# Performance work log

Measured on AMD Instinct MI355X. Metric: run time of the kernel, lower is better.

## Reference

```python
import jax, jax.numpy as jnp
import numpy as np

B, T, C, HEADS = 4, 2305, 384, 6
BN_EPS = 1e-5


def setup_inputs() -> dict:
    key = jax.random.key(0)
    ks = jax.random.split(key, 24)
    d = {
        'x': jax.random.normal(ks[0], (B, T, C), dtype=jnp.float32),
        'h': 48,
        'w': 48,
        # depthwise conv kernels (groups=C, no bias): OIHW with I=1
        'kq': jax.random.normal(ks[1], (C, 1, 3, 3), dtype=jnp.float32) * 0.1,
        'kk': jax.random.normal(ks[2], (C, 1, 3, 3), dtype=jnp.float32) * 0.1,
        'kv': jax.random.normal(ks[3], (C, 1, 3, 3), dtype=jnp.float32) * 0.1,
        # BatchNorm (eval mode) params per projection: gamma, beta, running_mean, running_var
        'gq': jax.random.normal(ks[4], (C,), dtype=jnp.float32) * 0.1 + 1.0,
        'bq': jax.random.normal(ks[5], (C,), dtype=jnp.float32) * 0.1,
        'mq': jax.random.normal(ks[6], (C,), dtype=jnp.float32) * 0.1,
        'vq': jax.random.uniform(ks[7], (C,), dtype=jnp.float32) + 0.5,
        'gk': jax.random.normal(ks[8], (C,), dtype=jnp.float32) * 0.1 + 1.0,
        'bk': jax.random.normal(ks[9], (C,), dtype=jnp.float32) * 0.1,
        'mk': jax.random.normal(ks[10], (C,), dtype=jnp.float32) * 0.1,
        'vk': jax.random.uniform(ks[11], (C,), dtype=jnp.float32) + 0.5,
        'gv': jax.random.normal(ks[12], (C,), dtype=jnp.float32) * 0.1 + 1.0,
        'bv': jax.random.normal(ks[13], (C,), dtype=jnp.float32) * 0.1,
        'mv': jax.random.normal(ks[14], (C,), dtype=jnp.float32) * 0.1,
        'vv': jax.random.uniform(ks[15], (C,), dtype=jnp.float32) + 0.5,
        # Linear weights, torch convention [out, in]; qkv_bias=False
        'Wq': jax.random.normal(ks[16], (C, C), dtype=jnp.float32) / np.sqrt(C),
        'Wk': jax.random.normal(ks[17], (C, C), dtype=jnp.float32) / np.sqrt(C),
        'Wv': jax.random.normal(ks[18], (C, C), dtype=jnp.float32) / np.sqrt(C),
        'Wo': jax.random.normal(ks[19], (C, C), dtype=jnp.float32) / np.sqrt(C),
        'bo': jax.random.normal(ks[20], (C,), dtype=jnp.float32) * 0.01,
    }
    return d


def _dw_bn(xi, kern, gamma, beta, mean, var, h, w):
    # xi: [B, C, h, w]; depthwise 3x3 conv, stride 1, pad 1, then eval-mode BN
    y = jax.lax.conv_general_dilated(
        xi, kern, window_strides=(1, 1), padding=((1, 1), (1, 1)),
        feature_group_count=C, dimension_numbers=('NCHW', 'OIHW', 'NCHW'))
    scale = (gamma / jnp.sqrt(var + BN_EPS))[None, :, None, None]
    y = (y - mean[None, :, None, None]) * scale + beta[None, :, None, None]
    # b c h w -> b (h w) c
    return y.transpose(0, 2, 3, 1).reshape(y.shape[0], h * w, C)


def _forward(x, kq, kk, kv, gq, bq, mq, vq, gk, bk, mk, vk, gv, bv, mv, vv,
             Wq, Wk, Wv, Wo, bo, h, w):
    b, t, c = x.shape
    scale = c ** (-0.5)  # note: dim**-0.5, NOT head_dim**-0.5 (as in source)
    cls_tok, xs = x[:, :1], x[:, 1:]
    xi = xs.reshape(b, h, w, c).transpose(0, 3, 1, 2)  # b (h w) c -> b c h w
    q = jnp.concatenate([cls_tok, _dw_bn(xi, kq, gq, bq, mq, vq, h, w)], axis=1)
    k = jnp.concatenate([cls_tok, _dw_bn(xi, kk, gk, bk, mk, vk, h, w)], axis=1)
    v = jnp.concatenate([cls_tok, _dw_bn(xi, kv, gv, bv, mv, vv, h, w)], axis=1)
    dh = c // HEADS
    q = (q @ Wq.T).reshape(b, t, HEADS, dh).transpose(0, 2, 1, 3)  # bhtd
    k = (k @ Wk.T).reshape(b, t, HEADS, dh).transpose(0, 2, 1, 3)
    v = (v @ Wv.T).reshape(b, t, HEADS, dh).transpose(0, 2, 1, 3)
    attn = jax.nn.softmax(jnp.einsum('bhld,bhtd->bhlt', q, k) * scale, axis=-1)
    out = jnp.einsum('bhlt,bhtd->bhld', attn, v)
    out = out.transpose(0, 2, 1, 3).reshape(b, t, c)
    return out @ Wo.T + bo


def reference(x, kq, kk, kv, gq, bq, mq, vq, gk, bk, mk, vk, gv, bv, mv, vv,
              Wq, Wk, Wv, Wo, bo, h, w):
    return _forward(x, kq, kk, kv, gq, bq, mq, vq, gk, bk, mk, vk, gv, bv,
                    mv, vv, Wq, Wk, Wv, Wo, bo, h, w)
```

## Files before the change

### kernel.cpp

```cpp
#include <hip/hip_runtime.h>
#include <hip/hip_bf16.h>

#define BN 4
#define TT 2305
#define CC 384
#define HH 6
#define DH 64
#define GW 48
#define BH (BN*HH)
#define TP 2368
#define TQP 2560
#define MF 9220
#define MP 9344
#define MB2 73
#define NSPL 2
#define C2 0.07362223f

typedef __hip_bfloat16 bf16;
typedef __attribute__((ext_vector_type(8))) short short8;
typedef __attribute__((ext_vector_type(4))) float floatx4;
typedef __attribute__((ext_vector_type(16))) float floatx16;

#define MFMA16(a,b,c) __builtin_amdgcn_mfma_f32_16x16x32_bf16((a),(b),(c),0,0,0)
#define MFMA32(a,b,c) __builtin_amdgcn_mfma_f32_32x32x16_bf16((a),(b),(c),0,0,0)

__device__ __forceinline__ unsigned pack2(float a, float b) {
    bf16 lo = __float2bfloat16(a);
    bf16 hi = __float2bfloat16(b);
    unsigned short ul = *reinterpret_cast<unsigned short*>(&lo);
    unsigned short uh = *reinterpret_cast<unsigned short*>(&hi);
    return (unsigned)ul | ((unsigned)uh << 16);
}
__device__ __forceinline__ float bu2f(unsigned u16) {
    unsigned v = u16 << 16;
    return *reinterpret_cast<float*>(&v);
}

__global__ __launch_bounds__(384)
void conv_bn(const float* __restrict__ x,
             const float* __restrict__ kq, const float* __restrict__ kk, const float* __restrict__ kv,
             const float* __restrict__ gq, const float* __restrict__ bq, const float* __restrict__ mq, const float* __restrict__ vq,
             const float* __restrict__ gk, const float* __restrict__ bk, const float* __restrict__ mk, const float* __restrict__ vk,
             const float* __restrict__ gv, const float* __restrict__ bv, const float* __restrict__ mv, const float* __restrict__ vv,
             const float* __restrict__ Wq, const float* __restrict__ Wk,
             const float* __restrict__ Wv, const float* __restrict__ Wo,
             bf16* __restrict__ wqb, bf16* __restrict__ wkb,
             bf16* __restrict__ wvb, bf16* __restrict__ wob,
             bf16* __restrict__ cq, bf16* __restrict__ ck, bf16* __restrict__ cv)
{
    {
        const int i = blockIdx.x * 384 + threadIdx.x;
        if (i < CC * CC) {
            wqb[i] = __float2bfloat16(Wq[i]);
            wkb[i] = __float2bfloat16(Wk[i]);
            wvb[i] = __float2bfloat16(Wv[i]);
            wob[i] = __float2bfloat16(Wo[i]);
        }
    }

    const int n = blockIdx.x;
    const int b = n / 289;
    const int idx = n % 289;
    const int c = threadIdx.x;
    const size_t xbase = (size_t)b * TT * CC;

    if (idx == 288) {
        bf16 xv = __float2bfloat16(x[xbase + c]);
        const size_t mrow = (size_t)(b * TT) * CC + c;
        cq[mrow] = xv; ck[mrow] = xv; cv[mrow] = xv;
        return;
    }

    const float sq = gq[c] * rsqrtf(vq[c] + 1e-5f), oq = bq[c] - mq[c] * sq;
    const float sk = gk[c] * rsqrtf(vk[c] + 1e-5f), ok = bk[c] - mk[c] * sk;
    const float sv = gv[c] * rsqrtf(vv[c] + 1e-5f), ov = bv[c] - mv[c] * sv;
    float wq9[9], wk9[9], wv9[9];
    #pragma unroll
    for (int u = 0; u < 9; u++) {
        wq9[u] = kq[c * 9 + u]; wk9[u] = kk[c * 9 + u]; wv9[u] = kv[c * 9 + u];
    }

    const int i = idx / 6;
    const int j0 = (idx % 6) * 8;

    float win[3][10];
    #pragma unroll
    for (int di = 0; di < 3; di++) {
        const int ii = i + di - 1;
        const bool rowok = (ii >= 0) && (ii < GW);
        #pragma unroll
        for (int wj = 0; wj < 10; wj++) {
            const int jj = j0 - 1 + wj;
            win[di][wj] = (rowok && jj >= 0 && jj < GW)
                ? x[xbase + (size_t)(1 + ii * GW + jj) * CC + c] : 0.f;
        }
    }

    #pragma unroll
    for (int g = 0; g < 8; g++) {
        float aq = 0.f, ak = 0.f, av = 0.f;
        #pragma unroll
        for (int di = 0; di < 3; di++)
            #pragma unroll
            for (int dj = 0; dj < 3; dj++) {
                const float xv = win[di][g + dj];
                const int u = di * 3 + dj;
                aq += xv * wq9[u]; ak += xv * wk9[u]; av += xv * wv9[u];
            }
        const int t = 1 + i * GW + j0 + g;
        const size_t mrow = (size_t)(b * TT + t) * CC + c;
        cq[mrow] = __float2bfloat16(aq * sq + oq);
        ck[mrow] = __float2bfloat16(ak * sk + ok);
        cv[mrow] = __float2bfloat16(av * sv + ov);
    }
}

__global__ __launch_bounds__(256)
void qkv_gemm(const bf16* __restrict__ cq, const bf16* __restrict__ ck, const bf16* __restrict__ cv,
              const bf16* __restrict__ Wq, const bf16* __restrict__ Wk, const bf16* __restrict__ Wv,
              bf16* __restrict__ q, bf16* __restrict__ k, bf16* __restrict__ vT)
{
    const int bt = blockIdx.x;
    const int b = bt / 10;
    const int m0 = (bt % 10) * 256;
    const int n0 = blockIdx.y * 64;
    const int w = threadIdx.x >> 6, lane = threadIdx.x & 63;
    const int lm = lane & 15, q4 = lane >> 4;
    const int which = n0 / CC;
    const int obase = n0 % CC;
    const bf16* A = (which == 0) ? cq : (which == 1) ? ck : cv;
    const bf16* W = (which == 0) ? Wq : (which == 1) ? Wk : Wv;

    __shared__ __align__(16) bf16 TR[64 * 264];

    size_t arow[4];
    #pragma unroll
    for (int st = 0; st < 4; st++) {
        int t = m0 + st * 64 + w * 16 + lm;
        if (t >= TT) t = TT - 1;
        arow[st] = (size_t)(b * TT + t) * CC;
    }

    floatx4 acc[4][4];
    #pragma unroll
    for (int st = 0; st < 4; st++)
        #pragma unroll
        for (int n = 0; n < 4; n++) acc[st][n] = (floatx4){0.f, 0.f, 0.f, 0.f};

    #pragma unroll 2
    for (int kc = 0; kc < CC / 32; kc++) {
        short8 a[4];
        #pragma unroll
        for (int st = 0; st < 4; st++)
            a[st] = *(const short8*)(A + arow[st] + kc * 32 + q4 * 8);
        #pragma unroll
        for (int n = 0; n < 4; n++) {
            short8 bfr = *(const short8*)(W + (size_t)(obase + n * 16 + lm) * CC + kc * 32 + q4 * 8);
            #pragma unroll
            for (int st = 0; st < 4; st++)
                acc[st][n] = MFMA16(a[st], bfr, acc[st][n]);
        }
    }

    if (which == 2) {
        #pragma unroll
        for (int st = 0; st < 4; st++)
            #pragma unroll
            for (int n = 0; n < 4; n++) {
                const int ol = n * 16 + lm;
                const int ml = st * 64 + w * 16 + q4 * 4;
                uint2 pkd = { pack2(acc[st][n][0], acc[st][n][1]),
                              pack2(acc[st][n][2], acc[st][n][3]) };
                *(uint2*)&TR[ol * 264 + ml] = pkd;
            }
        __syncthreads();
        const int h = obase >> 6;
        const int o = threadIdx.x >> 2;
        const int seg = threadIdx.x & 3;
        const size_t vrow = ((size_t)(b * HH + h) * DH + o) * TP;
        #pragma unroll
        for (int j = 0; j < 8; j++) {
            const int ml = seg * 64 + j * 8;
            const int t = m0 + ml;
            uint4 val = *(const uint4*)&TR[o * 264 + ml];
            if (t + 8 <= TT) {
                *(uint4*)(vT + vrow + t) = val;
            } else if (t < TT) {
                const bf16* pv = (const bf16*)&val;
                for (int e = 0; e < 8 && t + e < TT; e++) vT[vrow + t + e] = pv[e];
            }
        }
    } else {
        #pragma unroll
        for (int st = 0; st < 4; st++)
            #pragma unroll
            for (int n = 0; n < 4; n++) {
                const int o = obase + n * 16 + lm;
                const int h = o >> 6, d = o & 63;
                #pragma unroll
                for (int r = 0; r < 4; r++) {
                    const int t = m0 + st * 64 + w * 16 + q4 * 4 + r;
                    if (t >= TT) continue;
                    bf16 val = __float2bfloat16(acc[st][n][r]);
                    if (which == 0)
                        q[((size_t)(b * HH + h) * TQP + t) * DH + d] = val;
                    else
                        k[((size_t)(b * HH + h) * TP + t) * DH + d] = val;
                }
            }
    }
}

__global__ __launch_bounds__(256, 2)
void flash(const bf16* __restrict__ q, const bf16* __restrict__ k,
           const bf16* __restrict__ vT, bf16* __restrict__ OP, float* __restrict__ ML)
{
    const int id = blockIdx.x;
    const int bh = id % BH;
    const int rest = id / BH;
    const int z = rest % NSPL;
    const int qt = rest / NSPL;
    const int tid = threadIdx.x;
    const int w = tid >> 6, lane = tid & 63;
    const int q31 = lane & 31, hh = lane >> 5;
    const int q0 = qt * 256 + w * 64;
    const size_t kbase = (size_t)bh * TP * DH;
    const size_t qbase = (size_t)bh * TQP * DH;

    short8 qf[2][4];
    #pragma unroll
    for (int s = 0; s < 2; s++) {
        int qr = q0 + s * 32 + q31;
        if (qr > TT - 1) qr = TT - 1;
        const bf16* qrow = q + qbase + (size_t)qr * DH;
        #pragma unroll
        for (int kc = 0; kc < 4; kc++)
            qf[s][kc] = *(const short8*)(qrow + kc * 16 + hh * 8);
    }

    floatx16 of[2][2];
    #pragma unroll
    for (int s = 0; s < 2; s++)
        #pragma unroll
        for (int dt = 0; dt < 2; dt++)
            #pragma unroll
            for (int r = 0; r < 16; r++) of[s][dt][r] = 0.f;
    float m2[2] = {-1e30f, -1e30f}, lsum[2] = {0.f, 0.f};

    const int tstart = z ? 19 : 0;
    const int tend   = z ? 37 : 19;

    for (int tc = tstart; tc < tend; tc++) {
        const int t0 = tc * 64;
        const bf16* kt = k + kbase + (size_t)t0 * DH;
        const bf16* vt = vT + kbase + t0;

        short8 ka[2][4], va[2][4];
        #pragma unroll
        for (int mt = 0; mt < 2; mt++)
            #pragma unroll
            for (int kc = 0; kc < 4; kc++) {
                const int row = mt * 32 + q31, c = 2 * kc + hh;
                ka[mt][kc] = *(const short8*)(kt + (size_t)row * DH + c * 8);
                va[mt][kc] = *(const short8*)(vt + (size_t)row * TP + c * 8);
            }
        const bool tail = (t0 + 64 > TT);

        #pragma unroll
        for (int s = 0; s < 2; s++) {
            floatx16 sv[2];
            #pragma unroll
            for (int mt = 0; mt < 2; mt++)
                #pragma unroll
                for (int r = 0; r < 16; r++) sv[mt][r] = 0.f;
            __builtin_amdgcn_s_setprio(1);
            #pragma unroll
            for (int kc = 0; kc < 4; kc++) {
                sv[0] = MFMA32(ka[0][kc], qf[s][kc], sv[0]);
                sv[1] = MFMA32(ka[1][kc], qf[s][kc], sv[1]);
            }
            __builtin_amdgcn_s_setprio(0);
            if (tail) {
                #pragma unroll
                for (int mt = 0; mt < 2; mt++)
                    #pragma unroll
                    for (int r = 0; r < 16; r++) {
                        const int tl = t0 + mt * 32 + (r & 3) + 8 * (r >> 2) + 4 * hh;
                        if (tl >= TT) sv[mt][r] = -1e30f;
                    }
            }
            float r8[8];
            #pragma unroll
            for (int p = 0; p < 8; p++)
                r8[p] = fmaxf(fmaxf(sv[0][2 * p], sv[0][2 * p + 1]),
                              fmaxf(sv[1][2 * p], sv[1][2 * p + 1]));
            float rm = fmaxf(fmaxf(fmaxf(r8[0], r8[1]), fmaxf(r8[2], r8[3])),
                             fmaxf(fmaxf(r8[4], r8[5]), fmaxf(r8[6], r8[7])));
            rm = fmaxf(rm, __shfl_xor(rm, 32));
            const float rms = rm * C2;

            if (!__all(rms <= m2[s] + 8.f)) {
                const float mn = fmaxf(m2[s], rms);
                const float alpha = __builtin_amdgcn_exp2f(m2[s] - mn);
                m2[s] = mn;
                lsum[s] *= alpha;
                #pragma unroll
                for (int dt = 0; dt < 2; dt++)
                    #pragma unroll
                    for (int r = 0; r < 16; r++) of[s][dt][r] *= alpha;
            }
            const float negm = -m2[s];

            float rsp[4] = {0.f, 0.f, 0.f, 0.f};
            unsigned pk[2][8];
            #pragma unroll
            for (int mt = 0; mt < 2; mt++)
                #pragma unroll
                for (int p = 0; p < 8; p++) {
                    const float p0 = __builtin_amdgcn_exp2f(fmaf(sv[mt][2 * p], C2, negm));
                    const float p1 = __builtin_amdgcn_exp2f(fmaf(sv[mt][2 * p + 1], C2, negm));
                    rsp[p & 3] += p0 + p1;
                    pk[mt][p] = pack2(p0, p1);
                }
            float rs = (rsp[0] + rsp[1]) + (rsp[2] + rsp[3]);
            rs += __shfl_xor(rs, 32);
            lsum[s] += rs;

            #pragma unroll
            for (int kc = 0; kc < 4; kc++) {
                const int u0 = 2 * kc, u1 = 2 * kc + 1;
                const unsigned P0a = pk[u0 >> 2][2 * (u0 & 3)];
                const unsigned P0b = pk[u0 >> 2][2 * (u0 & 3) + 1];
                const unsigned P1a = pk[u1 >> 2][2 * (u1 & 3)];
                const unsigned P1b = pk[u1 >> 2][2 * (u1 & 3) + 1];
                const unsigned X1 = hh ? P0a : P1a;
                const unsigned X2 = hh ? P0b : P1b;
                const unsigned Y1 = __shfl_xor(X1, 32);
                const unsigned Y2 = __shfl_xor(X2, 32);
                unsigned dw[4];
                dw[0] = hh ? Y1 : P0a;
                dw[1] = hh ? Y2 : P0b;
                dw[2] = hh ? P1a : Y1;
                dw[3] = hh ? P1b : Y2;
                short8 pb = *reinterpret_cast<short8*>(dw);
                __builtin_amdgcn_s_setprio(1);
                of[s][0] = MFMA32(va[0][kc], pb, of[s][0]);
                of[s][1] = MFMA32(va[1][kc], pb, of[s][1]);
                __builtin_amdgcn_s_setprio(0);
            }
        }
    }

    #pragma unroll
    for (int s = 0; s < 2; s++) {
        const int qrow = q0 + s * 32 + q31;
        if (qrow >= TT) continue;
        bf16* orow = OP + ((size_t)(z * BH + bh) * TT + qrow) * DH;
        #pragma unroll
        for (int dt = 0; dt < 2; dt++)
            #pragma unroll
            for (int p = 0; p < 4; p++) {
                const int d = dt * 32 + 8 * p + 4 * hh;
                unsigned lo = pack2(of[s][dt][4 * p], of[s][dt][4 * p + 1]);
                unsigned hi = pack2(of[s][dt][4 * p + 2], of[s][dt][4 * p + 3]);
                uint2 st = {lo, hi};
                *(uint2*)(orow + d) = st;
            }
        if (hh == 0) {
            float2 ml = {m2[s], lsum[s]};
            *(float2*)&ML[((size_t)(z * BH + bh) * TT + qrow) * 2] = ml;
        }
    }
}

__global__ __launch_bounds__(256)
void merge(const bf16* __restrict__ OP, const float* __restrict__ ML,
           bf16* __restrict__ att)
{
    const int idx = blockIdx.x * 256 + threadIdx.x;
    if (idx >= BH * TT * 16) return;
    const int quad = idx & 15;
    const int pair = idx >> 4;
    const int bh = pair / TT, row = pair % TT;
    const int b = bh / HH, h = bh % HH;
    const int d0 = quad * 4;

    float2 ml[NSPL];
    #pragma unroll
    for (int z = 0; z < NSPL; z++)
        ml[z] = *(const float2*)&ML[((size_t)(z * BH + bh) * TT + row) * 2];
    float M = ml[0].x;
    #pragma unroll
    for (int z = 1; z < NSPL; z++) M = fmaxf(M, ml[z].x);
    float wz[NSPL], den = 0.f;
    #pragma unroll
    for (int z = 0; z < NSPL; z++) {
        wz[z] = __builtin_amdgcn_exp2f(ml[z].x - M);
        den += ml[z].y * wz[z];
    }
    const float inv = 1.f / den;

    float o0 = 0.f, o1 = 0.f, o2 = 0.f, o3 = 0.f;
    #pragma unroll
    for (int z = 0; z < NSPL; z++) {
        const float s = wz[z] * inv;
        const uint2 a = *(const uint2*)&OP[((size_t)(z * BH + bh) * TT + row) * DH + d0];
        o0 += bu2f(a.x & 0xffffu) * s;
        o1 += bu2f(a.x >> 16)     * s;
        o2 += bu2f(a.y & 0xffffu) * s;
        o3 += bu2f(a.y >> 16)     * s;
    }
    uint2 st = {pack2(o0, o1), pack2(o2, o3)};
    *(uint2*)&att[((size_t)(b * TT + row) * CC) + h * DH + d0] = st;
}

__global__ __launch_bounds__(256)
void out_gemm(const bf16* __restrict__ att, const bf16* __restrict__ Wo_bf,
              const float* __restrict__ bo, float* __restrict__ out)
{
    const int m0 = blockIdx.x * 128;
    const int n0 = blockIdx.y * 64;
    const int w = threadIdx.x >> 6, lane = threadIdx.x & 63;
    const int lm = lane & 15, q4 = lane >> 4;

    const size_t ar0 = (size_t)(m0 + w * 16 + lm) * CC;
    floatx4 acc[2][4];
    #pragma unroll
    for (int st = 0; st < 2; st++)
        #pragma unroll
        for (int n = 0; n < 4; n++) acc[st][n] = (floatx4){0.f, 0.f, 0.f, 0.f};

    #pragma unroll 4
    for (int kc = 0; kc < CC / 32; kc++) {
        short8 a0 = *(const short8*)(att + ar0 + kc * 32 + q4 * 8);
        short8 a1 = *(const short8*)(att + ar0 + (size_t)64 * CC + kc * 32 + q4 * 8);
        #pragma unroll
        for (int n = 0; n < 4; n++) {
            short8 bfr = *(const short8*)(Wo_bf + (size_t)(n0 + n * 16 + lm) * CC + kc * 32 + q4 * 8);
            acc[0][n] = MFMA16(a0, bfr, acc[0][n]);
            acc[1][n] = MFMA16(a1, bfr, acc[1][n]);
        }
    }

    #pragma unroll
    for (int st = 0; st < 2; st++)
        #pragma unroll
        for (int n = 0; n < 4; n++) {
            const int o = n0 + n * 16 + lm;
            const float bias = bo[o];
            #pragma unroll
            for (int r = 0; r < 4; r++) {
                const int m = m0 + st * 64 + w * 16 + q4 * 4 + r;
                if (m < MF) out[(size_t)m * CC + o] = acc[st][n][r] + bias;
            }
        }
}

extern "C" void kernel_launch(void* const* d_in, const int* in_sizes, int n_in,
                              void* d_out, int out_size, void* d_ws, size_t ws_size,
                              hipStream_t stream)
{
    const float* x  = (const float*)d_in[0];
    const float* kq = (const float*)d_in[3];
    const float* kk = (const float*)d_in[4];
    const float* kv = (const float*)d_in[5];
    const float* gq = (const float*)d_in[6];
    const float* bq = (const float*)d_in[7];
    const float* mq = (const float*)d_in[8];
    const float* vq = (const float*)d_in[9];
    const float* gk = (const float*)d_in[10];
    const float* bk = (const float*)d_in[11];
    const float* mk = (const float*)d_in[12];
    const float* vk = (const float*)d_in[13];
    const float* gv = (const float*)d_in[14];
    const float* bv = (const float*)d_in[15];
    const float* mv = (const float*)d_in[16];
    const float* vv = (const float*)d_in[17];
    const float* Wq = (const float*)d_in[18];
    const float* Wk = (const float*)d_in[19];
    const float* Wv = (const float*)d_in[20];
    const float* Wo = (const float*)d_in[21];
    const float* bo = (const float*)d_in[22];

    char* ws = (char*)d_ws;
    const size_t SZ_CONV = (size_t)MP * CC * 2;
    const size_t SZ_Q    = (size_t)BH * TQP * DH * 2;
    const size_t SZ_K    = (size_t)BH * TP * DH * 2;
    const size_t SZ_W    = (size_t)CC * CC * 2;
    size_t off = 0;
    bf16* cq   = (bf16*)(ws + off); off += SZ_CONV;
    bf16* ck   = (bf16*)(ws + off); off += SZ_CONV;
    bf16* cv   = (bf16*)(ws + off); off += SZ_CONV;
    bf16* qb   = (bf16*)(ws + off); off += SZ_Q;
    bf16* kb   = (bf16*)(ws + off); off += SZ_K;
    bf16* vTb  = (bf16*)(ws + off); off += SZ_K;
    bf16* attb = (bf16*)(ws + off); off += SZ_CONV;
    bf16* wqb  = (bf16*)(ws + off); off += SZ_W;
    bf16* wkb  = (bf16*)(ws + off); off += SZ_W;
    bf16* wvb  = (bf16*)(ws + off); off += SZ_W;
    bf16* wob  = (bf16*)(ws + off); off += SZ_W;
    bf16*  OP = (bf16*)ws;
    float* ML = (float*)(ws + off); off += (size_t)NSPL * BH * TT * 2 * 4;

    conv_bn<<<BN * 289, 384, 0, stream>>>(x, kq, kk, kv,
                                          gq, bq, mq, vq,
                                          gk, bk, mk, vk,
                                          gv, bv, mv, vv,
                                          Wq, Wk, Wv, Wo,
                                          wqb, wkb, wvb, wob,
                                          cq, ck, cv);
    qkv_gemm<<<dim3(40, 18), 256, 0, stream>>>(cq, ck, cv, wqb, wkb, wvb, qb, kb, vTb);
    flash<<<10 * NSPL * BH, 256, 0, stream>>>(qb, kb, vTb, OP, ML);
    merge<<<(BH * TT * 16 + 255) / 256, 256, 0, stream>>>(OP, ML, attb);
    out_gemm<<<dim3(MB2, 6), 256, 0, stream>>>(attb, wob, bo, (float*)d_out);
}
```

Before: 274.3 us.

## Process query sub-tiles sequentially in flash kernel to cut registers, raise occupancy

The flash kernel now loops over its two 32-row query sub-tiles one after the other instead of interleaving them inside the key loop. This halves the live accumulator and Q-fragment registers, and the launch bound goes from 2 to 3 blocks per CU. The V loads are moved after the QK MFMAs. In exchange, every K and V tile is loaded twice per wave instead of once, which doubles global and L2 load traffic, and each wave has less independent MFMA work to hide latency.

```diff
diff --git a/kernel.cpp b/kernel.cpp
--- a/kernel.cpp
+++ b/kernel.cpp
@@ -211,7 +211,7 @@
     }
 }
 
-__global__ __launch_bounds__(256, 2)
+__global__ __launch_bounds__(256, 3)
 void flash(const bf16* __restrict__ q, const bf16* __restrict__ k,
            const bf16* __restrict__ vT, bf16* __restrict__ OP, float* __restrict__ ML)
 {
@@ -227,47 +227,40 @@
     const size_t kbase = (size_t)bh * TP * DH;
     const size_t qbase = (size_t)bh * TQP * DH;
 
-    short8 qf[2][4];
-    #pragma unroll
+    const int tstart = z ? 19 : 0;
+    const int tend   = z ? 37 : 19;
+
+    #pragma unroll 1
     for (int s = 0; s < 2; s++) {
         int qr = q0 + s * 32 + q31;
         if (qr > TT - 1) qr = TT - 1;
-        const bf16* qrow = q + qbase + (size_t)qr * DH;
-        #pragma unroll
-        for (int kc = 0; kc < 4; kc++)
-            qf[s][kc] = *(const short8*)(qrow + kc * 16 + hh * 8);
-    }
-
-    floatx16 of[2][2];
-    #pragma unroll
-    for (int s = 0; s < 2; s++)
+        short8 qf[4];
+        {
+            const bf16* qrow = q + qbase + (size_t)qr * DH;
+            #pragma unroll
+            for (int kc = 0; kc < 4; kc++)
+                qf[kc] = *(const short8*)(qrow + kc * 16 + hh * 8);
+        }
+
+        floatx16 of[2];
         #pragma unroll
         for (int dt = 0; dt < 2; dt++)
             #pragma unroll
-            for (int r = 0; r < 16; r++) of[s][dt][r] = 0.f;
-    float m2[2] = {-1e30f, -1e30f}, lsum[2] = {0.f, 0.f};
-
-    const int tstart = z ? 19 : 0;
-    const int tend   = z ? 37 : 19;
-
-    for (int tc = tstart; tc < tend; tc++) {
-        const int t0 = tc * 64;
-        const bf16* kt = k + kbase + (size_t)t0 * DH;
-        const bf16* vt = vT + kbase + t0;
-
-        short8 ka[2][4], va[2][4];
-        #pragma unroll
-        for (int mt = 0; mt < 2; mt++)
-            #pragma unroll
-            for (int kc = 0; kc < 4; kc++) {
-                const int row = mt * 32 + q31, c = 2 * kc + hh;
-                ka[mt][kc] = *(const short8*)(kt + (size_t)row * DH + c * 8);
-                va[mt][kc] = *(const short8*)(vt + (size_t)row * TP + c * 8);
-            }
-        const bool tail = (t0 + 64 > TT);
-
-        #pragma unroll
-        for (int s = 0; s < 2; s++) {
+            for (int r = 0; r < 16; r++) of[dt][r] = 0.f;
+        float m2 = -1e30f, lsum = 0.f;
+
+        for (int tc = tstart; tc < tend; tc++) {
+            const int t0 = tc * 64;
+            const bf16* kt = k + kbase + (size_t)t0 * DH;
+            const bf16* vt = vT + kbase + t0;
+
+            short8 ka[2][4];
+            #pragma unroll
+            for (int mt = 0; mt < 2; mt++)
+                #pragma unroll
+                for (int kc = 0; kc < 4; kc++)
+                    ka[mt][kc] = *(const short8*)(kt + (size_t)(mt * 32 + q31) * DH + (2 * kc + hh) * 8);
+
             floatx16 sv[2];
             #pragma unroll
             for (int mt = 0; mt < 2; mt++)
@@ -276,11 +269,19 @@
             __builtin_amdgcn_s_setprio(1);
             #pragma unroll
             for (int kc = 0; kc < 4; kc++) {
-                sv[0] = MFMA32(ka[0][kc], qf[s][kc], sv[0]);
-                sv[1] = MFMA32(ka[1][kc], qf[s][kc], sv[1]);
+                sv[0] = MFMA32(ka[0][kc], qf[kc], sv[0]);
+                sv[1] = MFMA32(ka[1][kc], qf[kc], sv[1]);
             }
             __builtin_amdgcn_s_setprio(0);
-            if (tail) {
+
+            short8 va[2][4];
+            #pragma unroll
+            for (int mt = 0; mt < 2; mt++)
+                #pragma unroll
+                for (int kc = 0; kc < 4; kc++)
+                    va[mt][kc] = *(const short8*)(vt + (size_t)(mt * 32 + q31) * TP + (2 * kc + hh) * 8);
+
+            if (t0 + 64 > TT) {
                 #pragma unroll
                 for (int mt = 0; mt < 2; mt++)
                     #pragma unroll
@@ -289,6 +290,7 @@
                         if (tl >= TT) sv[mt][r] = -1e30f;
                     }
             }
+
             float r8[8];
             #pragma unroll
             for (int p = 0; p < 8; p++)
@@ -299,17 +301,17 @@
             rm = fmaxf(rm, __shfl_xor(rm, 32));
             const float rms = rm * C2;
 
-            if (!__all(rms <= m2[s] + 8.f)) {
-                const float mn = fmaxf(m2[s], rms);
-                const float alpha = __builtin_amdgcn_exp2f(m2[s] - mn);
-                m2[s] = mn;
-                lsum[s] *= alpha;
+            if (!__all(rms <= m2 + 8.f)) {
+                const float mn = fmaxf(m2, rms);
+                const float alpha = __builtin_amdgcn_exp2f(m2 - mn);
+                m2 = mn;
+                lsum *= alpha;
                 #pragma unroll
                 for (int dt = 0; dt < 2; dt++)
                     #pragma unroll
-                    for (int r = 0; r < 16; r++) of[s][dt][r] *= alpha;
-            }
-            const float negm = -m2[s];
+                    for (int r = 0; r < 16; r++) of[dt][r] *= alpha;
+            }
+            const float negm = -m2;
 
             float rsp[4] = {0.f, 0.f, 0.f, 0.f};
             unsigned pk[2][8];
@@ -324,7 +326,7 @@
                 }
             float rs = (rsp[0] + rsp[1]) + (rsp[2] + rsp[3]);
             rs += __shfl_xor(rs, 32);
-            lsum[s] += rs;
+            lsum += rs;
 
             #pragma unroll
             for (int kc = 0; kc < 4; kc++) {
@@ -344,31 +346,29 @@
                 dw[3] = hh ? P1b : Y2;
                 short8 pb = *reinterpret_cast<short8*>(dw);
                 __builtin_amdgcn_s_setprio(1);
-                of[s][0] = MFMA32(va[0][kc], pb, of[s][0]);
-                of[s][1] = MFMA32(va[1][kc], pb, of[s][1]);
+                of[0] = MFMA32(va[0][kc], pb, of[0]);
+                of[1] = MFMA32(va[1][kc], pb, of[1]);
                 __builtin_amdgcn_s_setprio(0);
             }
         }
-    }
-
-    #pragma unroll
-    for (int s = 0; s < 2; s++) {
-        const int qrow = q0 + s * 32 + q31;
-        if (qrow >= TT) continue;
-        bf16* orow = OP + ((size_t)(z * BH + bh) * TT + qrow) * DH;
-        #pragma unroll
-        for (int dt = 0; dt < 2; dt++)
-            #pragma unroll
-            for (int p = 0; p < 4; p++) {
-                const int d = dt * 32 + 8 * p + 4 * hh;
-                unsigned lo = pack2(of[s][dt][4 * p], of[s][dt][4 * p + 1]);
-                unsigned hi = pack2(of[s][dt][4 * p + 2], of[s][dt][4 * p + 3]);
-                uint2 st = {lo, hi};
-                *(uint2*)(orow + d) = st;
-            }
-        if (hh == 0) {
-            float2 ml = {m2[s], lsum[s]};
-            *(float2*)&ML[((size_t)(z * BH + bh) * TT + qrow) * 2] = ml;
+
+        const int qrow_s = q0 + s * 32 + q31;
+        if (qrow_s < TT) {
+            bf16* orow = OP + ((size_t)(z * BH + bh) * TT + qrow_s) * DH;
+            #pragma unroll
+            for (int dt = 0; dt < 2; dt++)
+                #pragma unroll
+                for (int p = 0; p < 4; p++) {
+                    const int d = dt * 32 + 8 * p + 4 * hh;
+                    unsigned lo = pack2(of[dt][4 * p], of[dt][4 * p + 1]);
+                    unsigned hi = pack2(of[dt][4 * p + 2], of[dt][4 * p + 3]);
+                    uint2 st = {lo, hi};
+                    *(uint2*)(orow + d) = st;
+                }
+            if (hh == 0) {
+                float2 ml = {m2, lsum};
+                *(float2*)&ML[((size_t)(z * BH + bh) * TT + qrow_s) * 2] = ml;
+            }
         }
     }
 }
```

After: 330.9 us. +20.6%, slower.

## Stage K/V tiles through double-buffered LDS with register prefetch in flash kernel

Applied to the files above, without the earlier changes.

The flash attention kernel now loads each 64-row K and V^T tile cooperatively into padded shared-memory buffers. The next tile is prefetched into registers while the current one is computed, then written to the alternate buffer, with one barrier per iteration. This replaces the previous pattern where each of the four waves fetched the whole K/V tile straight from global memory, so global traffic is shared across waves and load latency overlaps compute. In exchange it adds about 35 KB of LDS per block and a __syncthreads each iteration, which may limit occupancy at two blocks per CU.

```diff
diff --git a/kernel.cpp b/kernel.cpp
--- a/kernel.cpp
+++ b/kernel.cpp
@@ -14,6 +14,7 @@
 #define MP 9344
 #define MB2 73
 #define NSPL 2
+#define QTI 10
 #define C2 0.07362223f
 
 typedef __hip_bfloat16 bf16;
@@ -227,6 +228,15 @@
     const size_t kbase = (size_t)bh * TP * DH;
     const size_t qbase = (size_t)bh * TQP * DH;
 
+    __shared__ __align__(16) bf16 Kl[2][64][68];
+    __shared__ __align__(16) bf16 Vl[2][64][68];
+
+    const int srow = tid >> 3;
+    const int scol = (tid & 7) * 8;
+
+    const int tstart = z ? 19 : 0;
+    const int tend   = z ? 37 : 19;
+
     short8 qf[2][4];
     #pragma unroll
     for (int s = 0; s < 2; s++) {
@@ -247,22 +257,43 @@
             for (int r = 0; r < 16; r++) of[s][dt][r] = 0.f;
     float m2[2] = {-1e30f, -1e30f}, lsum[2] = {0.f, 0.f};
 
-    const int tstart = z ? 19 : 0;
-    const int tend   = z ? 37 : 19;
-
+    {
+        const bf16* kt = k + kbase + (size_t)tstart * 64 * DH;
+        const bf16* vt = vT + kbase + tstart * 64;
+        uint4 kr0 = *(const uint4*)(kt + (size_t)srow * DH + scol);
+        uint4 kr1 = *(const uint4*)(kt + (size_t)(srow + 32) * DH + scol);
+        uint4 vr0 = *(const uint4*)(vt + (size_t)srow * TP + scol);
+        uint4 vr1 = *(const uint4*)(vt + (size_t)(srow + 32) * TP + scol);
+        *(uint4*)&Kl[0][srow][scol]      = kr0;
+        *(uint4*)&Kl[0][srow + 32][scol] = kr1;
+        *(uint4*)&Vl[0][srow][scol]      = vr0;
+        *(uint4*)&Vl[0][srow + 32][scol] = vr1;
+    }
+    __syncthreads();
+
+    int cur = 0;
+    #pragma unroll 1
     for (int tc = tstart; tc < tend; tc++) {
         const int t0 = tc * 64;
-        const bf16* kt = k + kbase + (size_t)t0 * DH;
-        const bf16* vt = vT + kbase + t0;
+        const bool have_next = (tc + 1 < tend);
+
+        uint4 kr0, kr1, vr0, vr1;
+        if (have_next) {
+            const bf16* kt = k + kbase + (size_t)(t0 + 64) * DH;
+            const bf16* vt = vT + kbase + (t0 + 64);
+            kr0 = *(const uint4*)(kt + (size_t)srow * DH + scol);
+            kr1 = *(const uint4*)(kt + (size_t)(srow + 32) * DH + scol);
+            vr0 = *(const uint4*)(vt + (size_t)srow * TP + scol);
+            vr1 = *(const uint4*)(vt + (size_t)(srow + 32) * TP + scol);
+        }
 
         short8 ka[2][4], va[2][4];
         #pragma unroll
         for (int mt = 0; mt < 2; mt++)
             #pragma unroll
             for (int kc = 0; kc < 4; kc++) {
-                const int row = mt * 32 + q31, c = 2 * kc + hh;
-                ka[mt][kc] = *(const short8*)(kt + (size_t)row * DH + c * 8);
-                va[mt][kc] = *(const short8*)(vt + (size_t)row * TP + c * 8);
+                ka[mt][kc] = *(const short8*)&Kl[cur][mt * 32 + q31][(2 * kc + hh) * 8];
+                va[mt][kc] = *(const short8*)&Vl[cur][mt * 32 + q31][(2 * kc + hh) * 8];
             }
         const bool tail = (t0 + 64 > TT);
 
@@ -349,6 +380,15 @@
                 __builtin_amdgcn_s_setprio(0);
             }
         }
+
+        if (have_next) {
+            *(uint4*)&Kl[cur ^ 1][srow][scol]      = kr0;
+            *(uint4*)&Kl[cur ^ 1][srow + 32][scol] = kr1;
+            *(uint4*)&Vl[cur ^ 1][srow][scol]      = vr0;
+            *(uint4*)&Vl[cur ^ 1][srow + 32][scol] = vr1;
+        }
+        __syncthreads();
+        cur ^= 1;
     }
 
     #pragma unroll
@@ -510,7 +550,7 @@
                                           wqb, wkb, wvb, wob,
                                           cq, ck, cv);
     qkv_gemm<<<dim3(40, 18), 256, 0, stream>>>(cq, ck, cv, wqb, wkb, wvb, qb, kb, vTb);
-    flash<<<10 * NSPL * BH, 256, 0, stream>>>(qb, kb, vTb, OP, ML);
+    flash<<<QTI * NSPL * BH, 256, 0, stream>>>(qb, kb, vTb, OP, ML);
     merge<<<(BH * TT * 16 + 255) / 256, 256, 0, stream>>>(OP, ML, attb);
     out_gemm<<<dim3(MB2, 6), 256, 0, stream>>>(attb, wob, bo, (float*)d_out);
 }
```

Result: faster. 250.3 us (-8.8%).
